# Kernel optimization log

Measured on AMD Instinct MI355X. Metric: run time of the kernel, lower is better.

## Reference

```python
import jax, jax.numpy as jnp
import numpy as np

TOTAL_DIM = 64  # 16+16+16+8+8
HIDDEN = 4 * TOTAL_DIM
NUM_HEADS = 8


def _fourier(x, num_freqs):
    # Dyadic Fourier features: sin/cos of 2^j * x for j in [0, num_freqs).
    # Output dim = input_dim * num_freqs * 2 (matches embed_dim in the module).
    freqs = 2.0 ** jnp.arange(num_freqs, dtype=x.dtype)  # (F,)
    phase = x[..., :, None] * freqs                       # (..., in, F)
    out = jnp.concatenate([jnp.sin(phase), jnp.cos(phase)], axis=-1)  # (..., in, 2F)
    return out.reshape(x.shape[:-1] + (-1,))


def setup_inputs() -> dict:
    key = jax.random.key(0)
    k1, k2, k3, k4, k5, k6 = jax.random.split(key, 6)
    B, Nq, Nk, D = 8, 256, 256, 10
    query_states = jax.random.normal(k1, (B, Nq, D), dtype=jnp.float32)
    key_states = jax.random.normal(k2, (B, Nk, D), dtype=jnp.float32)
    W1 = jax.random.normal(k3, (TOTAL_DIM, HIDDEN), dtype=jnp.float32) / np.sqrt(TOTAL_DIM)
    b1 = jnp.zeros((HIDDEN,), dtype=jnp.float32)
    W2 = jax.random.normal(k4, (HIDDEN, NUM_HEADS), dtype=jnp.float32) / np.sqrt(HIDDEN)
    b2 = jnp.zeros((NUM_HEADS,), dtype=jnp.float32)
    return {"query_states": query_states, "key_states": key_states,
            "W1": W1, "b1": b1, "W2": W2, "b2": b2}


def _features(query_states, key_states):
    # Slice per-ship fields, then broadcast pairwise: q -> (B,Nq,1,*), k -> (B,1,Nk,*)
    q_team = query_states[:, :, None, 0]          # (B,Nq,1)
    k_team = key_states[:, None, :, 0]            # (B,1,Nk)
    q_pos = query_states[:, :, None, 3:5]
    k_pos = key_states[:, None, :, 3:5]
    q_vel = query_states[:, :, None, 5:7]
    k_vel = key_states[:, None, :, 5:7]
    q_att = query_states[:, :, None, 7:9]
    k_att = key_states[:, None, :, 7:9]

    delta_pos = k_pos - q_pos                     # (B,Nq,Nk,2)
    delta_vel = k_vel - q_vel                     # (B,Nq,Nk,2)
    feat_delta_input = jnp.concatenate([delta_pos, delta_vel], axis=-1)  # (B,Nq,Nk,4)

    dist_sq = jnp.sum(delta_pos ** 2, axis=-1, keepdims=True)
    dist = jnp.sqrt(dist_sq + 1e-6)
    inv_dist = 1.0 / (dist + 0.1)
    feat_dist_input = jnp.concatenate([dist, inv_dist], axis=-1)         # (B,Nq,Nk,2)

    bearing = delta_pos / (dist + 1e-6)
    ata = jnp.sum(bearing * q_att, axis=-1, keepdims=True)
    aspect = jnp.sum(bearing * k_att, axis=-1, keepdims=True)
    feat_angle_input = jnp.concatenate([ata, aspect], axis=-1)           # (B,Nq,Nk,2)

    dot_dp_dv = jnp.sum(delta_pos * delta_vel, axis=-1, keepdims=True)
    speed_sq = jnp.sum(delta_vel ** 2, axis=-1, keepdims=True)
    ttca = jnp.tanh(jax.nn.relu(-dot_dp_dv / (speed_sq + 1e-6)))
    feat_intercept_input = jnp.concatenate([ttca, dist], axis=-1)        # (B,Nq,Nk,2)

    same_team = (q_team == k_team).astype(query_states.dtype)[..., None]
    q_speed = jnp.linalg.norm(q_vel, axis=-1, keepdims=True)
    k_speed = jnp.linalg.norm(k_vel, axis=-1, keepdims=True)
    delta_speed = k_speed - q_speed
    feat_team_input = jnp.concatenate([same_team, delta_speed], axis=-1)  # (B,Nq,Nk,2)

    out_dist = _fourier(feat_dist_input, 4)        # 16
    out_angle = _fourier(feat_angle_input, 4)      # 16
    out_delta = _fourier(feat_delta_input, 2)      # 16
    out_intercept = _fourier(feat_intercept_input, 2)  # 8
    out_team = _fourier(feat_team_input, 2)        # 8
    return jnp.concatenate([out_dist, out_angle, out_delta, out_intercept, out_team], axis=-1)


def reference(query_states, key_states, W1, b1, W2, b2):
    combined = _features(query_states, key_states)          # (B,Nq,Nk,64)
    h = jax.nn.silu(combined @ W1 + b1)                     # (B,Nq,Nk,256)
    bias = h @ W2 + b2                                      # (B,Nq,Nk,H)
    return jnp.transpose(bias, (0, 3, 1, 2))                # (B,H,Nq,Nk)
```

## Files before the change

kernel.cpp:

```cpp
#include <hip/hip_runtime.h>
#include <math.h>

#define NB 8
#define NQ 256
#define NK 256
#define DIN 10
#define FDIM 64
#define HIDDEN 256
#define NH 8
#define ROWS_PER_BLK 4

#define FSTRIDE 64
#define HSTRIDE 264
#define W2S 264

typedef float f32x4 __attribute__((ext_vector_type(4)));
typedef short bf16x8 __attribute__((ext_vector_type(8)));

__device__ __forceinline__ short f2bf(float f) {
    return (short)((__float_as_uint(f) + 0x8000u) >> 16);
}
__device__ __forceinline__ unsigned pack2(float a, float b) {
    unsigned ua = __float_as_uint(a) + 0x8000u;
    unsigned ub = __float_as_uint(b) + 0x8000u;
    return __builtin_amdgcn_perm(ub, ua, 0x07060302);
}

__device__ __forceinline__ void four4(float x, float* dst) {
    float s1 = __sinf(x), c1 = __cosf(x);
    float s2 = 2.f * s1 * c1, c2 = 1.f - 2.f * s1 * s1;
    float s4 = 2.f * s2 * c2, c4 = 1.f - 2.f * s2 * s2;
    float s8 = 2.f * s4 * c4, c8 = 1.f - 2.f * s4 * s4;
    dst[0] = s1; dst[1] = s2; dst[2] = s4; dst[3] = s8;
    dst[4] = c1; dst[5] = c2; dst[6] = c4; dst[7] = c8;
}
__device__ __forceinline__ void four2(float x, float* dst) {
    float s1 = __sinf(x), c1 = __cosf(x);
    dst[0] = s1; dst[1] = 2.f * s1 * c1;
    dst[2] = c1; dst[3] = 1.f - 2.f * s1 * s1;
}

__global__ __launch_bounds__(256, 2) void relfeat_mfma_kernel(
    const float* __restrict__ q, const float* __restrict__ k,
    const float* __restrict__ W1, const float* __restrict__ b1,
    const float* __restrict__ W2, const float* __restrict__ b2,
    float* __restrict__ out)
{
    __shared__ __align__(16) short feat_s[NK * FSTRIDE];
    __shared__ __align__(16) short h_s[64 * HSTRIDE];
    __shared__ __align__(16) short w2_s[8 * W2S];

    const int t = threadIdx.x;
    const int wave = t >> 6;
    const int lane15 = t & 15;
    const int quad = (t >> 4) & 3;
    const int b = blockIdx.x >> 6;
    const int i0 = (blockIdx.x & 63) * ROWS_PER_BLK;

    const float* kp = k + ((size_t)b * NK + t) * DIN;
    const float k0 = kp[0], k3 = kp[3], k4 = kp[4], k5 = kp[5], k6 = kp[6],
                k7 = kp[7], k8 = kp[8];

#pragma unroll
    for (int o = 0; o < NH; ++o)
        w2_s[o * W2S + t] = f2bf(-0.69314718f * W2[t * NH + o]);

    const int n0 = wave * 64;
    bf16x8 w1f[4][2];
#pragma unroll
    for (int nt = 0; nt < 4; ++nt)
#pragma unroll
        for (int ks = 0; ks < 2; ++ks) {
            const float* wp = W1 + (size_t)(ks * 32 + quad * 8) * HIDDEN
                              + (n0 + nt * 16 + lane15);
            bf16x8 v;
#pragma unroll
            for (int e = 0; e < 8; ++e)
                v[e] = f2bf(-1.44269504f * wp[(size_t)e * HIDDEN]);
            w1f[nt][ks] = v;
        }
    float4 b1q[4];
#pragma unroll
    for (int nt = 0; nt < 4; ++nt) {
        float4 bb = *(const float4*)&b1[n0 + nt * 16 + quad * 4];
        b1q[nt] = make_float4(-1.44269504f * bb.x, -1.44269504f * bb.y,
                              -1.44269504f * bb.z, -1.44269504f * bb.w);
    }
    const float b2v = (lane15 < NH) ? b2[lane15] : 0.f;

    const int sw = t & 7;
    const int swr = lane15 & 7;

#pragma unroll 1
    for (int row = 0; row < ROWS_PER_BLK; ++row) {
        const int i = i0 + row;

        {
            const float* qp = q + ((size_t)b * NQ + i) * DIN;
            const float q0 = qp[0], q3 = qp[3], q4 = qp[4], q5 = qp[5],
                        q6 = qp[6], q7 = qp[7], q8 = qp[8];

            const float dpx = k3 - q3, dpy = k4 - q4;
            const float dvx = k5 - q5, dvy = k6 - q6;
            const float dist = sqrtf(dpx * dpx + dpy * dpy + 1e-6f);
            const float inv_dist = 1.0f / (dist + 0.1f);
            const float inv_d2 = 1.0f / (dist + 1e-6f);
            const float bear_x = dpx * inv_d2, bear_y = dpy * inv_d2;
            const float ata = bear_x * q7 + bear_y * q8;
            const float aspect = bear_x * k7 + bear_y * k8;
            const float dot_dp_dv = dpx * dvx + dpy * dvy;
            const float speed_sq = dvx * dvx + dvy * dvy;
            const float ttca = tanhf(fmaxf(0.f, -dot_dp_dv / (speed_sq + 1e-6f)));
            const float same_team = (q0 == k0) ? 1.f : 0.f;
            const float q_speed = sqrtf(q5 * q5 + q6 * q6);
            const float k_speed = sqrtf(k5 * k5 + k6 * k6);
            const float delta_speed = k_speed - q_speed;

            float feat[FDIM];
            four4(dist,        feat + 0);
            four4(inv_dist,    feat + 8);
            four4(ata,         feat + 16);
            four4(aspect,      feat + 24);
            four2(dpx,         feat + 32);
            four2(dpy,         feat + 36);
            four2(dvx,         feat + 40);
            four2(dvy,         feat + 44);
            four2(ttca,        feat + 48);
            four2(dist,        feat + 52);
            four2(same_team,   feat + 56);
            four2(delta_speed, feat + 60);

#pragma unroll
            for (int c8 = 0; c8 < 8; ++c8) {
                uint4 v;
                v.x = pack2(feat[c8 * 8 + 0], feat[c8 * 8 + 1]);
                v.y = pack2(feat[c8 * 8 + 2], feat[c8 * 8 + 3]);
                v.z = pack2(feat[c8 * 8 + 4], feat[c8 * 8 + 5]);
                v.w = pack2(feat[c8 * 8 + 6], feat[c8 * 8 + 7]);
                *(uint4*)&feat_s[t * FSTRIDE + ((c8 ^ sw) * 8)] = v;
            }
        }
        __syncthreads();

#pragma unroll 1
        for (int c = 0; c < 4; ++c) {
            const int p0 = c * 64;

            f32x4 acc[4][4];
#pragma unroll
            for (int nt = 0; nt < 4; ++nt)
#pragma unroll
                for (int mt = 0; mt < 4; ++mt)
                    acc[nt][mt] = (f32x4){b1q[nt].x, b1q[nt].y, b1q[nt].z, b1q[nt].w};
#pragma unroll
            for (int ks = 0; ks < 2; ++ks)
#pragma unroll
                for (int mt = 0; mt < 4; ++mt) {
                    const int r2 = p0 + mt * 16 + lane15;
                    const bf16x8 fb = *(const bf16x8*)
                        &feat_s[r2 * FSTRIDE + (((ks * 4 + quad) ^ swr) * 8)];
#pragma unroll
                    for (int nt = 0; nt < 4; ++nt)
                        acc[nt][mt] = __builtin_amdgcn_mfma_f32_16x16x32_bf16(
                            w1f[nt][ks], fb, acc[nt][mt], 0, 0, 0);
                }

            __syncthreads();

#pragma unroll
            for (int nt = 0; nt < 4; ++nt)
#pragma unroll
                for (int mt = 0; mt < 4; ++mt) {
                    const int pair = mt * 16 + lane15;
                    const int hbase = n0 + nt * 16 + quad * 4;
                    float s[4];
#pragma unroll
                    for (int r = 0; r < 4; ++r) {
                        const float a = acc[nt][mt][r];
                        const float e = __builtin_amdgcn_exp2f(a);
                        s[r] = a * __builtin_amdgcn_rcpf(1.f + e);
                    }
                    uint2 pk;
                    pk.x = pack2(s[0], s[1]);
                    pk.y = pack2(s[2], s[3]);
                    *(uint2*)&h_s[pair * HSTRIDE + hbase] = pk;
                }
            __syncthreads();

            {
                const int pw = wave * 16;
                f32x4 acc2 = (f32x4){b2v, b2v, b2v, b2v};
#pragma unroll
                for (int ks = 0; ks < 8; ++ks) {
                    const bf16x8 ha = *(const bf16x8*)&h_s[(pw + lane15) * HSTRIDE
                                                            + ks * 32 + quad * 8];
                    const bf16x8 wb = *(const bf16x8*)&w2_s[(lane15 & 7) * W2S
                                                             + ks * 32 + quad * 8];
                    acc2 = __builtin_amdgcn_mfma_f32_16x16x32_bf16(ha, wb, acc2, 0, 0, 0);
                }
                if (lane15 < NH) {
                    float* op = out + (((size_t)b * NH + lane15) * NQ + i) * NK
                                + (p0 + pw + quad * 4);
                    *(float4*)op = make_float4(acc2[0], acc2[1], acc2[2], acc2[3]);
                }
            }
        }
    }
}

extern "C" void kernel_launch(void* const* d_in, const int* in_sizes, int n_in,
                              void* d_out, int out_size, void* d_ws, size_t ws_size,
                              hipStream_t stream) {
    const float* q  = (const float*)d_in[0];
    const float* k  = (const float*)d_in[1];
    const float* W1 = (const float*)d_in[2];
    const float* b1 = (const float*)d_in[3];
    const float* W2 = (const float*)d_in[4];
    const float* b2 = (const float*)d_in[5];
    float* out = (float*)d_out;

    dim3 grid(NB * NQ / ROWS_PER_BLK);
    dim3 block(NK);
    relfeat_mfma_kernel<<<grid, block, 0, stream>>>(q, k, W1, b1, W2, b2, out);
}
```

Before: 113.7 us.

## Double block size to 512 threads, splitting feature and hidden work across halves

Launches 512-thread blocks. Each half of the block computes a different subset of the 64 Fourier features per key, and each of the 8 waves owns 32 hidden units instead of 64. The same-team features become constants, and the duplicated dist features are reused rather than recomputed. The aim is more waves per CU to hide latency and less per-thread transcendental work, at the cost of an idle second-stage MFMA for half the waves and heavier barrier use.

```diff
diff --git a/kernel.cpp b/kernel.cpp
--- a/kernel.cpp
+++ b/kernel.cpp
@@ -40,7 +40,7 @@
     dst[2] = c1; dst[3] = 1.f - 2.f * s1 * s1;
 }
 
-__global__ __launch_bounds__(256, 2) void relfeat_mfma_kernel(
+__global__ __launch_bounds__(512, 4) void relfeat_mfma_kernel(
     const float* __restrict__ q, const float* __restrict__ k,
     const float* __restrict__ W1, const float* __restrict__ b1,
     const float* __restrict__ W2, const float* __restrict__ b2,
@@ -54,21 +54,25 @@
     const int wave = t >> 6;
     const int lane15 = t & 15;
     const int quad = (t >> 4) & 3;
+    const int p = t & 255;
+    const int half = t >> 8;
     const int b = blockIdx.x >> 6;
     const int i0 = (blockIdx.x & 63) * ROWS_PER_BLK;
 
-    const float* kp = k + ((size_t)b * NK + t) * DIN;
+    const float* kp = k + ((size_t)b * NK + p) * DIN;
     const float k0 = kp[0], k3 = kp[3], k4 = kp[4], k5 = kp[5], k6 = kp[6],
                 k7 = kp[7], k8 = kp[8];
 
 #pragma unroll
-    for (int o = 0; o < NH; ++o)
-        w2_s[o * W2S + t] = f2bf(-0.69314718f * W2[t * NH + o]);
-
-    const int n0 = wave * 64;
-    bf16x8 w1f[4][2];
-#pragma unroll
-    for (int nt = 0; nt < 4; ++nt)
+    for (int o2 = 0; o2 < 4; ++o2) {
+        const int o = half * 4 + o2;
+        w2_s[o * W2S + p] = f2bf(-0.69314718f * W2[p * NH + o]);
+    }
+
+    const int n0 = wave * 32;
+    bf16x8 w1f[2][2];
+#pragma unroll
+    for (int nt = 0; nt < 2; ++nt)
 #pragma unroll
         for (int ks = 0; ks < 2; ++ks) {
             const float* wp = W1 + (size_t)(ks * 32 + quad * 8) * HIDDEN
@@ -79,16 +83,16 @@
                 v[e] = f2bf(-1.44269504f * wp[(size_t)e * HIDDEN]);
             w1f[nt][ks] = v;
         }
-    float4 b1q[4];
-#pragma unroll
-    for (int nt = 0; nt < 4; ++nt) {
+    float4 b1q[2];
+#pragma unroll
+    for (int nt = 0; nt < 2; ++nt) {
         float4 bb = *(const float4*)&b1[n0 + nt * 16 + quad * 4];
         b1q[nt] = make_float4(-1.44269504f * bb.x, -1.44269504f * bb.y,
                               -1.44269504f * bb.z, -1.44269504f * bb.w);
     }
     const float b2v = (lane15 < NH) ? b2[lane15] : 0.f;
 
-    const int sw = t & 7;
+    const int sw = p & 7;
     const int swr = lane15 & 7;
 
 #pragma unroll 1
@@ -103,41 +107,48 @@
             const float dpx = k3 - q3, dpy = k4 - q4;
             const float dvx = k5 - q5, dvy = k6 - q6;
             const float dist = sqrtf(dpx * dpx + dpy * dpy + 1e-6f);
-            const float inv_dist = 1.0f / (dist + 0.1f);
-            const float inv_d2 = 1.0f / (dist + 1e-6f);
-            const float bear_x = dpx * inv_d2, bear_y = dpy * inv_d2;
-            const float ata = bear_x * q7 + bear_y * q8;
-            const float aspect = bear_x * k7 + bear_y * k8;
-            const float dot_dp_dv = dpx * dvx + dpy * dvy;
-            const float speed_sq = dvx * dvx + dvy * dvy;
-            const float ttca = tanhf(fmaxf(0.f, -dot_dp_dv / (speed_sq + 1e-6f)));
-            const float same_team = (q0 == k0) ? 1.f : 0.f;
-            const float q_speed = sqrtf(q5 * q5 + q6 * q6);
-            const float k_speed = sqrtf(k5 * k5 + k6 * k6);
-            const float delta_speed = k_speed - q_speed;
-
-            float feat[FDIM];
-            four4(dist,        feat + 0);
-            four4(inv_dist,    feat + 8);
-            four4(ata,         feat + 16);
-            four4(aspect,      feat + 24);
-            four2(dpx,         feat + 32);
-            four2(dpy,         feat + 36);
-            four2(dvx,         feat + 40);
-            four2(dvy,         feat + 44);
-            four2(ttca,        feat + 48);
-            four2(dist,        feat + 52);
-            four2(same_team,   feat + 56);
-            four2(delta_speed, feat + 60);
-
-#pragma unroll
-            for (int c8 = 0; c8 < 8; ++c8) {
+
+            float feat[32];
+            if (half == 0) {
+                const float inv_dist = 1.0f / (dist + 0.1f);
+                const float dot_dp_dv = dpx * dvx + dpy * dvy;
+                const float speed_sq = dvx * dvx + dvy * dvy;
+                const float ttca = tanhf(fmaxf(0.f, -dot_dp_dv / (speed_sq + 1e-6f)));
+                const float q_speed = sqrtf(q5 * q5 + q6 * q6);
+                const float k_speed = sqrtf(k5 * k5 + k6 * k6);
+                const float delta_speed = k_speed - q_speed;
+                four4(dist,     feat + 0);
+                four4(inv_dist, feat + 8);
+                four2(ttca,     feat + 16);
+                feat[20] = feat[0]; feat[21] = feat[1];
+                feat[22] = feat[4]; feat[23] = feat[5];
+                const bool st = (q0 == k0);
+                feat[24] = st ? 0.84147098f : 0.f;
+                feat[25] = st ? 0.90929743f : 0.f;
+                feat[26] = st ? 0.54030231f : 1.f;
+                feat[27] = st ? -0.41614684f : 1.f;
+                four2(delta_speed, feat + 28);
+            } else {
+                const float inv_d2 = 1.0f / (dist + 1e-6f);
+                const float bear_x = dpx * inv_d2, bear_y = dpy * inv_d2;
+                const float ata = bear_x * q7 + bear_y * q8;
+                const float aspect = bear_x * k7 + bear_y * k8;
+                four4(ata,    feat + 0);
+                four4(aspect, feat + 8);
+                four2(dpx,    feat + 16);
+                four2(dpy,    feat + 20);
+                four2(dvx,    feat + 24);
+                four2(dvy,    feat + 28);
+            }
+#pragma unroll
+            for (int j = 0; j < 4; ++j) {
+                const int c8 = half ? (j + 2) : (j < 2 ? j : j + 4);
                 uint4 v;
-                v.x = pack2(feat[c8 * 8 + 0], feat[c8 * 8 + 1]);
-                v.y = pack2(feat[c8 * 8 + 2], feat[c8 * 8 + 3]);
-                v.z = pack2(feat[c8 * 8 + 4], feat[c8 * 8 + 5]);
-                v.w = pack2(feat[c8 * 8 + 6], feat[c8 * 8 + 7]);
-                *(uint4*)&feat_s[t * FSTRIDE + ((c8 ^ sw) * 8)] = v;
+                v.x = pack2(feat[j * 8 + 0], feat[j * 8 + 1]);
+                v.y = pack2(feat[j * 8 + 2], feat[j * 8 + 3]);
+                v.z = pack2(feat[j * 8 + 4], feat[j * 8 + 5]);
+                v.w = pack2(feat[j * 8 + 6], feat[j * 8 + 7]);
+                *(uint4*)&feat_s[p * FSTRIDE + ((c8 ^ sw) * 8)] = v;
             }
         }
         __syncthreads();
@@ -146,9 +157,9 @@
         for (int c = 0; c < 4; ++c) {
             const int p0 = c * 64;
 
-            f32x4 acc[4][4];
-#pragma unroll
-            for (int nt = 0; nt < 4; ++nt)
+            f32x4 acc[2][4];
+#pragma unroll
+            for (int nt = 0; nt < 2; ++nt)
 #pragma unroll
                 for (int mt = 0; mt < 4; ++mt)
                     acc[nt][mt] = (f32x4){b1q[nt].x, b1q[nt].y, b1q[nt].z, b1q[nt].w};
@@ -160,7 +171,7 @@
                     const bf16x8 fb = *(const bf16x8*)
                         &feat_s[r2 * FSTRIDE + (((ks * 4 + quad) ^ swr) * 8)];
 #pragma unroll
-                    for (int nt = 0; nt < 4; ++nt)
+                    for (int nt = 0; nt < 2; ++nt)
                         acc[nt][mt] = __builtin_amdgcn_mfma_f32_16x16x32_bf16(
                             w1f[nt][ks], fb, acc[nt][mt], 0, 0, 0);
                 }
@@ -168,7 +179,7 @@
             __syncthreads();
 
 #pragma unroll
-            for (int nt = 0; nt < 4; ++nt)
+            for (int nt = 0; nt < 2; ++nt)
 #pragma unroll
                 for (int mt = 0; mt < 4; ++mt) {
                     const int pair = mt * 16 + lane15;
@@ -187,7 +198,7 @@
                 }
             __syncthreads();
 
-            {
+            if (wave < 4) {
                 const int pw = wave * 16;
                 f32x4 acc2 = (f32x4){b2v, b2v, b2v, b2v};
 #pragma unroll
@@ -220,6 +231,6 @@
     float* out = (float*)d_out;
 
     dim3 grid(NB * NQ / ROWS_PER_BLK);
-    dim3 block(NK);
+    dim3 block(512);
     relfeat_mfma_kernel<<<grid, block, 0, stream>>>(q, k, W1, b1, W2, b2, out);
 }
```

Result: no change. 112.6 us (-1.0%).
